# Performance work log

Hardware: AMD Instinct MI355X
Metric: run time of the kernel (lower is better)

Reference implementation:

```python
import jax, jax.numpy as jnp
import numpy as np

N, E, D = 20000, 320000, 256
EPS = 1e-5


def setup_inputs() -> dict:
    key = jax.random.key(0)
    ks = jax.random.split(key, 12)
    s = 1.0 / np.sqrt(D)
    s2 = 1.0 / np.sqrt(2 * D)
    return {
        "node_embeddings": jax.random.normal(ks[0], (N, D), jnp.float32),
        "edge_index": jax.random.randint(ks[1], (2, E), 0, N, jnp.int64),
        "edge_embeddings": jax.random.normal(ks[2], (E, D), jnp.float32),
        # message MLP: Linear(D,D) -> GELU -> Linear(D,D)
        "W1m": jax.random.uniform(ks[3], (D, D), jnp.float32, -s, s),
        "b1m": jnp.zeros((D,), jnp.float32),
        "W2m": jax.random.uniform(ks[4], (D, D), jnp.float32, -s, s),
        "b2m": jnp.zeros((D,), jnp.float32),
        # update MLP: Linear(D,2D) -> GELU -> Linear(2D,D)
        "W1u": jax.random.uniform(ks[5], (D, 2 * D), jnp.float32, -s, s),
        "b1u": jnp.zeros((2 * D,), jnp.float32),
        "W2u": jax.random.uniform(ks[6], (2 * D, D), jnp.float32, -s2, s2),
        "b2u": jnp.zeros((D,), jnp.float32),
        # LayerNorm params
        "gamma": jnp.ones((D,), jnp.float32),
        "beta": jnp.zeros((D,), jnp.float32),
    }


def _layer_norm(x, gamma, beta):
    mu = jnp.mean(x, axis=-1, keepdims=True)
    var = jnp.mean(jnp.square(x - mu), axis=-1, keepdims=True)
    return (x - mu) * jax.lax.rsqrt(var + EPS) * gamma + beta


def reference(node_embeddings, edge_index, edge_embeddings,
              W1m, b1m, W2m, b2m, W1u, b1u, W2u, b2u, gamma, beta):
    src = edge_index[0]
    dst = edge_index[1]
    n = node_embeddings.shape[0]
    # gather + edge add + message MLP (exact erf GELU, as torch default)
    h = node_embeddings[src] + edge_embeddings           # [E, D]
    h = jax.nn.gelu(h @ W1m + b1m, approximate=False)
    messages = h @ W2m + b2m                             # [E, D]
    # scatter-mean aggregation
    agg = jax.ops.segment_sum(messages, dst, num_segments=n)  # [N, D]
    deg = jax.ops.segment_sum(jnp.ones((dst.shape[0], 1), node_embeddings.dtype),
                              dst, num_segments=n)            # [N, 1]
    agg = agg / jnp.maximum(deg, 1.0)
    # update MLP + residual + LayerNorm
    u = jax.nn.gelu(agg @ W1u + b1u, approximate=False) @ W2u + b2u
    return _layer_norm(node_embeddings + u, gamma, beta)
```

## Files before the change

### kernel.cpp

```cpp
#include <hip/hip_runtime.h>
#include <hip/hip_bf16.h>

#define N_NODES 20000
#define N_EDGES 320000

typedef __attribute__((ext_vector_type(8))) short short8;
typedef __attribute__((ext_vector_type(4))) float f32x4;

static __device__ __forceinline__ unsigned short f2bf(float f) {
  __hip_bfloat16 h = __float2bfloat16(f);
  union { __hip_bfloat16 h; unsigned short u; } cv; cv.h = h; return cv.u;
}

static __device__ __forceinline__ float bf2f(unsigned short u) {
  union { unsigned int u; float f; } cv; cv.u = ((unsigned int)u) << 16; return cv.f;
}

static __device__ __forceinline__ unsigned int pk2(float a, float b) {
  return (unsigned int)f2bf(a) | ((unsigned int)f2bf(b) << 16);
}

static __device__ __forceinline__ float gelu_exact(float v) {
  return 0.5f * v * (1.0f + erff(v * 0.70710678118654752f));
}

#define SWZ(row, byteoff) ((byteoff) ^ (((row) & 7) << 4))
#define SWZU(b) ((b) ^ ((((b) >> 8) & 7) << 4))

__global__ void zero_kernel(float4* __restrict__ S4, int4* __restrict__ cnt4) {
  int idx = blockIdx.x * blockDim.x + threadIdx.x;
  S4[idx] = make_float4(0.f, 0.f, 0.f, 0.f);
  if (idx < N_NODES / 4) cnt4[idx] = make_int4(0, 0, 0, 0);
}

__global__ void pack_kernel(const float* __restrict__ W1m, const float* __restrict__ W2m,
                            const float* __restrict__ W1u, const float* __restrict__ W2u,
                            unsigned short* __restrict__ P1m, unsigned short* __restrict__ P2m,
                            unsigned short* __restrict__ P1u, unsigned short* __restrict__ P2u) {
  int idx = blockIdx.x * blockDim.x + threadIdx.x;
  const float* W; unsigned short* P; int K, Nc, local;
  if (idx < 65536)        { W = W1m; P = P1m; K = 256; Nc = 256; local = idx; }
  else if (idx < 131072)  { W = W2m; P = P2m; K = 256; Nc = 256; local = idx - 65536; }
  else if (idx < 262144)  { W = W1u; P = P1u; K = 256; Nc = 512; local = idx - 131072; }
  else                    { W = W2u; P = P2u; K = 512; Nc = 256; local = idx - 262144; }
  int frag = local >> 9, wi = local & 511;
  int l = wi >> 3, i = wi & 7;
  int kf = K >> 5;
  int cf = frag / kf, t = frag % kf;
  int k = t * 32 + (l >> 4) * 8 + i;
  int n = cf * 16 + (l & 15);
  P[local] = f2bf(W[(size_t)k * Nc + n]);
}

__global__ void hist_kernel(const int* __restrict__ dst, int* __restrict__ cnt) {
  int e = blockIdx.x * blockDim.x + threadIdx.x;
  atomicAdd(&cnt[dst[e]], 1);
}

__global__ __launch_bounds__(1024) void scan_kernel(const int* __restrict__ cnt,
                                                    int* __restrict__ rptr,
                                                    int* __restrict__ cur) {
  __shared__ int sums[1024];
  const int t = threadIdx.x;
  const int base = t * 20;
  int local[20];
  int s = 0;
#pragma unroll
  for (int i = 0; i < 20; ++i) {
    int idx = base + i;
    int v = (idx < N_NODES) ? cnt[idx] : 0;
    local[i] = s;
    s += v;
  }
  int v = s;
  sums[t] = v;
  for (int off = 1; off < 1024; off <<= 1) {
    __syncthreads();
    int o = (t >= off) ? sums[t - off] : 0;
    __syncthreads();
    v += o;
    sums[t] = v;
  }
  int excl = v - s;
#pragma unroll
  for (int i = 0; i < 20; ++i) {
    int idx = base + i;
    if (idx < N_NODES) { int p = excl + local[i]; rptr[idx] = p; cur[idx] = p; }
  }
  if (t == 1023) rptr[N_NODES] = v;
}

__global__ void scatter_kernel(const int* __restrict__ dst, int* __restrict__ cur,
                               int* __restrict__ perm) {
  int e = blockIdx.x * blockDim.x + threadIdx.x;
  int d = dst[e];
  int pos = atomicAdd(&cur[d], 1);
  perm[pos] = e;
}

__global__ __launch_bounds__(256) void edge_kernel(
    const float* __restrict__ node, const float* __restrict__ eemb,
    const int* __restrict__ src, const int* __restrict__ dst,
    const int* __restrict__ perm,
    const unsigned short* __restrict__ P1m, const float* __restrict__ b1m,
    float* __restrict__ S) {
  __shared__ unsigned short tA[64 * 256];
  __shared__ int dstS[64];
  const int tid = threadIdx.x;
  const int e0 = blockIdx.x * 64;
  {
    const int r = tid >> 2;
    const int cs = (tid & 3) * 64;
    const int e = perm[e0 + r];
    const int se = src[e];
    if ((tid & 3) == 0) dstS[r] = dst[e];
    const float* ep = eemb + (size_t)e * 256 + cs;
    const float* np = node + (size_t)se * 256 + cs;
#pragma unroll
    for (int i = 0; i < 8; ++i) {
      float4 a = *(const float4*)(ep + i * 8);
      float4 b = *(const float4*)(np + i * 8);
      float4 c = *(const float4*)(ep + i * 8 + 4);
      float4 d = *(const float4*)(np + i * 8 + 4);
      uint4 p;
      p.x = pk2(a.x + b.x, a.y + b.y);
      p.y = pk2(a.z + b.z, a.w + b.w);
      p.z = pk2(c.x + d.x, c.y + d.y);
      p.w = pk2(c.z + d.z, c.w + d.w);
      *(uint4*)((char*)tA + SWZ(r, r * 512 + (cs + i * 8) * 2)) = p;
    }
  }
  __syncthreads();

  const int w = tid >> 6, l = tid & 63;
  const int lr = l & 15, lh = l >> 4;
  f32x4 acc[4][4];
#pragma unroll
  for (int c = 0; c < 4; ++c) {
    float bb = b1m[w * 64 + c * 16 + lr];
#pragma unroll
    for (int r4 = 0; r4 < 4; ++r4) acc[r4][c] = f32x4{bb, bb, bb, bb};
  }
#pragma unroll
  for (int t = 0; t < 8; ++t) {
    short8 af[4], bfr[4];
#pragma unroll
    for (int r4 = 0; r4 < 4; ++r4) {
      int row = r4 * 16 + lr;
      af[r4] = *(const short8*)((const char*)tA + SWZ(row, row * 512 + t * 64 + lh * 16));
    }
#pragma unroll
    for (int c = 0; c < 4; ++c)
      bfr[c] = *(const short8*)(P1m + (size_t)(((w * 4 + c) * 8 + t) * 512 + l * 8));
#pragma unroll
    for (int r4 = 0; r4 < 4; ++r4)
#pragma unroll
      for (int c = 0; c < 4; ++c)
        acc[r4][c] = __builtin_amdgcn_mfma_f32_16x16x32_bf16(af[r4], bfr[c], acc[r4][c], 0, 0, 0);
  }
  __syncthreads();

#pragma unroll
  for (int r4 = 0; r4 < 4; ++r4)
#pragma unroll
    for (int c = 0; c < 4; ++c) {
      int col = w * 64 + c * 16 + lr;
#pragma unroll
      for (int j = 0; j < 4; ++j) {
        int row = r4 * 16 + lh * 4 + j;
        *(unsigned short*)((char*)tA + SWZ(row, row * 512 + col * 2)) =
            f2bf(gelu_exact(acc[r4][c][j]));
      }
    }
  __syncthreads();

  {
    const int col = tid;
    float run = 0.f;
    int cur = dstS[0];
#pragma unroll 8
    for (int row = 0; row < 64; ++row) {
      int d = dstS[row];
      float v = bf2f(*(const unsigned short*)((const char*)tA + SWZ(row, row * 512 + col * 2)));
      if (d != cur) {
        atomicAdd(&S[(size_t)cur * 256 + col], run);
        run = 0.f;
        cur = d;
      }
      run += v;
    }
    atomicAdd(&S[(size_t)cur * 256 + col], run);
  }
}

__global__ __launch_bounds__(256) void node_kernel(
    const float* __restrict__ node, const float* __restrict__ S, const int* __restrict__ rptr,
    const unsigned short* __restrict__ P2m, const float* __restrict__ b2m,
    const unsigned short* __restrict__ P1u, const float* __restrict__ b1u,
    const unsigned short* __restrict__ P2u, const float* __restrict__ b2u,
    const float* __restrict__ gamma, const float* __restrict__ beta,
    float* __restrict__ out) {
  __shared__ unsigned short tAB[2][64 * 256];
  __shared__ unsigned short tH[64 * 512];
  __shared__ float fmu[64], frs[64], fflag[64];
  float* tU = (float*)tAB;
  const int tid = threadIdx.x;
  const int n0 = blockIdx.x * 64;
  const int r = tid >> 2;
  const int cs = (tid & 3) * 64;
  const int n = n0 + r;
  const bool valid = n < N_NODES;
  {
    int dgi = valid ? (rptr[n + 1] - rptr[n]) : 0;
    float dg = (float)dgi;
    float rec = 1.0f / fmaxf(dg, 1.0f);
    if ((tid & 3) == 0) fflag[r] = (dgi > 0) ? 1.0f : 0.0f;
    const float4* sp = (const float4*)(S + (size_t)n * 256 + cs);
#pragma unroll
    for (int i = 0; i < 8; ++i) {
      float4 a = valid ? sp[2 * i]     : make_float4(0.f, 0.f, 0.f, 0.f);
      float4 b = valid ? sp[2 * i + 1] : make_float4(0.f, 0.f, 0.f, 0.f);
      uint4 p;
      p.x = pk2(a.x * rec, a.y * rec);
      p.y = pk2(a.z * rec, a.w * rec);
      p.z = pk2(b.x * rec, b.y * rec);
      p.w = pk2(b.z * rec, b.w * rec);
      *(uint4*)((char*)tAB[0] + SWZ(r, r * 512 + (cs + i * 8) * 2)) = p;
    }
  }
  __syncthreads();
  const int w = tid >> 6, l = tid & 63, lr = l & 15, lh = l >> 4;

  {
    f32x4 acc[4][4];
#pragma unroll
    for (int r4 = 0; r4 < 4; ++r4)
#pragma unroll
      for (int c = 0; c < 4; ++c) acc[r4][c] = f32x4{0.f, 0.f, 0.f, 0.f};
#pragma unroll
    for (int t = 0; t < 8; ++t) {
      short8 af[4], bfr[4];
#pragma unroll
      for (int r4 = 0; r4 < 4; ++r4) {
        int row = r4 * 16 + lr;
        af[r4] = *(const short8*)((const char*)tAB[0] + SWZ(row, row * 512 + t * 64 + lh * 16));
      }
#pragma unroll
      for (int c = 0; c < 4; ++c)
        bfr[c] = *(const short8*)(P2m + (size_t)(((w * 4 + c) * 8 + t) * 512 + l * 8));
#pragma unroll
      for (int r4 = 0; r4 < 4; ++r4)
#pragma unroll
        for (int c = 0; c < 4; ++c)
          acc[r4][c] = __builtin_amdgcn_mfma_f32_16x16x32_bf16(af[r4], bfr[c], acc[r4][c], 0, 0, 0);
    }
#pragma unroll
    for (int r4 = 0; r4 < 4; ++r4)
#pragma unroll
      for (int c = 0; c < 4; ++c) {
        int col = w * 64 + c * 16 + lr;
        float bm = b2m[col];
#pragma unroll
        for (int j = 0; j < 4; ++j) {
          int row = r4 * 16 + lh * 4 + j;
          float v = acc[r4][c][j] + fflag[row] * bm;
          *(unsigned short*)((char*)tAB[1] + SWZ(row, row * 512 + col * 2)) = f2bf(v);
        }
      }
  }
  __syncthreads();

  {
    f32x4 acc[4][8];
#pragma unroll
    for (int r4 = 0; r4 < 4; ++r4)
#pragma unroll
      for (int c = 0; c < 8; ++c) acc[r4][c] = f32x4{0.f, 0.f, 0.f, 0.f};
#pragma unroll
    for (int t = 0; t < 8; ++t) {
      short8 af[4], bfr[8];
#pragma unroll
      for (int r4 = 0; r4 < 4; ++r4) {
        int row = r4 * 16 + lr;
        af[r4] = *(const short8*)((const char*)tAB[1] + SWZ(row, row * 512 + t * 64 + lh * 16));
      }
#pragma unroll
      for (int c = 0; c < 8; ++c)
        bfr[c] = *(const short8*)(P1u + (size_t)(((w * 8 + c) * 8 + t) * 512 + l * 8));
#pragma unroll
      for (int r4 = 0; r4 < 4; ++r4)
#pragma unroll
        for (int c = 0; c < 8; ++c)
          acc[r4][c] = __builtin_amdgcn_mfma_f32_16x16x32_bf16(af[r4], bfr[c], acc[r4][c], 0, 0, 0);
    }
#pragma unroll
    for (int r4 = 0; r4 < 4; ++r4)
#pragma unroll
      for (int c = 0; c < 8; ++c) {
        int col = w * 128 + c * 16 + lr;
        float b1 = b1u[col];
#pragma unroll
        for (int j = 0; j < 4; ++j) {
          int row = r4 * 16 + lh * 4 + j;
          float v = gelu_exact(acc[r4][c][j] + b1);
          *(unsigned short*)((char*)tH + SWZ(row, row * 1024 + col * 2)) = f2bf(v);
        }
      }
  }
  __syncthreads();

  {
    f32x4 acc[4][4];
#pragma unroll
    for (int r4 = 0; r4 < 4; ++r4)
#pragma unroll
      for (int c = 0; c < 4; ++c) acc[r4][c] = f32x4{0.f, 0.f, 0.f, 0.f};
#pragma unroll
    for (int t = 0; t < 16; ++t) {
      short8 af[4], bfr[4];
#pragma unroll
      for (int r4 = 0; r4 < 4; ++r4) {
        int row = r4 * 16 + lr;
        af[r4] = *(const short8*)((const char*)tH + SWZ(row, row * 1024 + t * 64 + lh * 16));
      }
#pragma unroll
      for (int c = 0; c < 4; ++c)
        bfr[c] = *(const short8*)(P2u + (size_t)(((w * 4 + c) * 16 + t) * 512 + l * 8));
#pragma unroll
      for (int r4 = 0; r4 < 4; ++r4)
#pragma unroll
        for (int c = 0; c < 4; ++c)
          acc[r4][c] = __builtin_amdgcn_mfma_f32_16x16x32_bf16(af[r4], bfr[c], acc[r4][c], 0, 0, 0);
    }
#pragma unroll
    for (int r4 = 0; r4 < 4; ++r4)
#pragma unroll
      for (int c = 0; c < 4; ++c) {
        int col = w * 64 + c * 16 + lr;
        float b2 = b2u[col];
#pragma unroll
        for (int j = 0; j < 4; ++j) {
          int row = r4 * 16 + lh * 4 + j;
          *(float*)((char*)tU + SWZU(row * 1024 + col * 4)) = acc[r4][c][j] + b2;
        }
      }
  }
  __syncthreads();

  {
    float sum = 0.f, sq = 0.f;
#pragma unroll
    for (int i = 0; i < 16; ++i) {
      int byte = SWZU(r * 1024 + (cs + i * 4) * 4);
      float4 v = *(float4*)((char*)tU + byte);
      if (valid) {
        const float4 nb = *(const float4*)(node + (size_t)n * 256 + cs + i * 4);
        v.x += nb.x; v.y += nb.y; v.z += nb.z; v.w += nb.w;
        *(float4*)((char*)tU + byte) = v;
      }
      sum += v.x + v.y + v.z + v.w;
      sq += v.x * v.x + v.y * v.y + v.z * v.z + v.w * v.w;
    }
    sum += __shfl_xor(sum, 1); sum += __shfl_xor(sum, 2);
    sq  += __shfl_xor(sq, 1);  sq  += __shfl_xor(sq, 2);
    if ((tid & 3) == 0) {
      float mu = sum * (1.0f / 256.0f);
      fmu[r] = mu;
      frs[r] = rsqrtf(fmaxf(sq * (1.0f / 256.0f) - mu * mu, 0.0f) + 1e-5f);
    }
  }
  __syncthreads();
#pragma unroll
  for (int i = 0; i < 16; ++i) {
    int f4 = i * 256 + tid;
    int row = f4 >> 6;
    int c4 = f4 & 63;
    int nn = n0 + row;
    if (nn < N_NODES) {
      float4 v = *(float4*)((char*)tU + SWZU(row * 1024 + c4 * 16));
      float mu = fmu[row], rs = frs[row];
      float4 g  = *(const float4*)(gamma + c4 * 4);
      float4 bt = *(const float4*)(beta + c4 * 4);
      float4 o;
      o.x = (v.x - mu) * rs * g.x + bt.x;
      o.y = (v.y - mu) * rs * g.y + bt.y;
      o.z = (v.z - mu) * rs * g.z + bt.z;
      o.w = (v.w - mu) * rs * g.w + bt.w;
      *(float4*)(out + (size_t)nn * 256 + c4 * 4) = o;
    }
  }
}

extern "C" void kernel_launch(void* const* d_in, const int* in_sizes, int n_in,
                              void* d_out, int out_size, void* d_ws, size_t ws_size,
                              hipStream_t stream) {
  const float* node = (const float*)d_in[0];
  const int* eidx = (const int*)d_in[1];
  const float* eemb = (const float*)d_in[2];
  const float* W1m = (const float*)d_in[3];
  const float* b1m = (const float*)d_in[4];
  const float* W2m = (const float*)d_in[5];
  const float* b2m = (const float*)d_in[6];
  const float* W1u = (const float*)d_in[7];
  const float* b1u = (const float*)d_in[8];
  const float* W2u = (const float*)d_in[9];
  const float* b2u = (const float*)d_in[10];
  const float* gamma = (const float*)d_in[11];
  const float* beta = (const float*)d_in[12];
  float* out = (float*)d_out;

  char* ws = (char*)d_ws;
  int* cnt  = (int*)ws;
  int* rptr = (int*)(ws + 81920);
  int* cur  = (int*)(ws + 163840);
  int* perm = (int*)(ws + 245760);
  unsigned short* P1m = (unsigned short*)(ws + 1525760);
  unsigned short* P2m = (unsigned short*)(ws + 1656832);
  unsigned short* P1u = (unsigned short*)(ws + 1787904);
  unsigned short* P2u = (unsigned short*)(ws + 2050048);
  const int* src = eidx;
  const int* dst = eidx + N_EDGES;

  zero_kernel<<<N_NODES * 64 / 256, 256, 0, stream>>>((float4*)out, (int4*)cnt);
  pack_kernel<<<393216 / 256, 256, 0, stream>>>(W1m, W2m, W1u, W2u, P1m, P2m, P1u, P2u);
  hist_kernel<<<N_EDGES / 256, 256, 0, stream>>>(dst, cnt);
  scan_kernel<<<1, 1024, 0, stream>>>(cnt, rptr, cur);
  scatter_kernel<<<N_EDGES / 256, 256, 0, stream>>>(dst, cur, perm);
  edge_kernel<<<N_EDGES / 64, 256, 0, stream>>>(node, eemb, src, dst, perm, P1m, b1m, out);
  node_kernel<<<(N_NODES + 63) / 64, 256, 0, stream>>>(node, out, rptr, P2m, b2m,
                                                       P1u, b1u, P2u, b2u, gamma, beta, out);
}
```

Before: 387.2 us.

## Software-pipeline edge tiles in edge_kernel and use fast exp-based GELU

Each edge block now processes four 64-edge tiles and prefetches the next tile's gathered node and edge rows into registers while the current tile runs its MFMA, GELU and scatter phases. This hides global gather latency and amortises per-block setup. It also replaces the exact erf GELU with a sigmoid-style exp2 and reciprocal approximation in both kernels, which is cheaper but slightly less accurate. The launch has a quarter as many blocks, which reduces parallelism, and extra registers are held for the staging buffers.

```diff
diff --git a/kernel.cpp b/kernel.cpp
--- a/kernel.cpp
+++ b/kernel.cpp
@@ -3,6 +3,7 @@
 
 #define N_NODES 20000
 #define N_EDGES 320000
+#define ETILES 4
 
 typedef __attribute__((ext_vector_type(8))) short short8;
 typedef __attribute__((ext_vector_type(4))) float f32x4;
@@ -20,8 +21,19 @@
   return (unsigned int)f2bf(a) | ((unsigned int)f2bf(b) << 16);
 }
 
-static __device__ __forceinline__ float gelu_exact(float v) {
-  return 0.5f * v * (1.0f + erff(v * 0.70710678118654752f));
+static __device__ __forceinline__ float gelu_f(float x) {
+  float z = x * (2.3022082f + 0.1029432f * x * x);
+  z = fminf(fmaxf(z, -30.0f), 30.0f);
+#if __has_builtin(__builtin_amdgcn_exp2f)
+  float t = __builtin_amdgcn_exp2f(z);
+#else
+  float t = exp2f(z);
+#endif
+#if __has_builtin(__builtin_amdgcn_rcpf)
+  return x * t * __builtin_amdgcn_rcpf(1.0f + t);
+#else
+  return x * t / (1.0f + t);
+#endif
 }
 
 #define SWZ(row, byteoff) ((byteoff) ^ (((row) & 7) << 4))
@@ -107,89 +119,122 @@
   __shared__ unsigned short tA[64 * 256];
   __shared__ int dstS[64];
   const int tid = threadIdx.x;
-  const int e0 = blockIdx.x * 64;
-  {
-    const int r = tid >> 2;
-    const int cs = (tid & 3) * 64;
-    const int e = perm[e0 + r];
-    const int se = src[e];
-    if ((tid & 3) == 0) dstS[r] = dst[e];
-    const float* ep = eemb + (size_t)e * 256 + cs;
-    const float* np = node + (size_t)se * 256 + cs;
-#pragma unroll
-    for (int i = 0; i < 8; ++i) {
-      float4 a = *(const float4*)(ep + i * 8);
-      float4 b = *(const float4*)(np + i * 8);
-      float4 c = *(const float4*)(ep + i * 8 + 4);
-      float4 d = *(const float4*)(np + i * 8 + 4);
-      uint4 p;
-      p.x = pk2(a.x + b.x, a.y + b.y);
-      p.y = pk2(a.z + b.z, a.w + b.w);
-      p.z = pk2(c.x + d.x, c.y + d.y);
-      p.w = pk2(c.z + d.z, c.w + d.w);
-      *(uint4*)((char*)tA + SWZ(r, r * 512 + (cs + i * 8) * 2)) = p;
-    }
-  }
-  __syncthreads();
-
-  const int w = tid >> 6, l = tid & 63;
-  const int lr = l & 15, lh = l >> 4;
-  f32x4 acc[4][4];
-#pragma unroll
-  for (int c = 0; c < 4; ++c) {
-    float bb = b1m[w * 64 + c * 16 + lr];
-#pragma unroll
-    for (int r4 = 0; r4 < 4; ++r4) acc[r4][c] = f32x4{bb, bb, bb, bb};
-  }
-#pragma unroll
-  for (int t = 0; t < 8; ++t) {
-    short8 af[4], bfr[4];
-#pragma unroll
-    for (int r4 = 0; r4 < 4; ++r4) {
-      int row = r4 * 16 + lr;
-      af[r4] = *(const short8*)((const char*)tA + SWZ(row, row * 512 + t * 64 + lh * 16));
-    }
+  const int r = tid >> 2, cs = (tid & 3) * 64;
+  const int w = tid >> 6, l = tid & 63, lr = l & 15, lh = l >> 4;
+  const int base = blockIdx.x * (64 * ETILES);
+
+  int eId[ETILES], sId[ETILES], dId[ETILES];
+#pragma unroll
+  for (int t = 0; t < ETILES; ++t) eId[t] = perm[base + t * 64 + r];
+#pragma unroll
+  for (int t = 0; t < ETILES; ++t) { sId[t] = src[eId[t]]; dId[t] = dst[eId[t]]; }
+
+  float bias_c[4];
+#pragma unroll
+  for (int c = 0; c < 4; ++c) bias_c[c] = b1m[w * 64 + c * 16 + lr];
+
+  float4 fa[8], fb[8];
+  uint4 stg[8];
+
+  auto issue_half = [&](int t, int h) {
+    const float* ep = eemb + (size_t)eId[t] * 256 + cs + h * 32;
+    const float* np = node + (size_t)sId[t] * 256 + cs + h * 32;
+#pragma unroll
+    for (int j = 0; j < 8; ++j) {
+      fa[j] = *(const float4*)(ep + j * 4);
+      fb[j] = *(const float4*)(np + j * 4);
+    }
+  };
+  auto pack_half = [&](uint4* o) {
+#pragma unroll
+    for (int j = 0; j < 4; ++j) {
+      float4 a = fa[2 * j], b = fb[2 * j], c = fa[2 * j + 1], d = fb[2 * j + 1];
+      o[j].x = pk2(a.x + b.x, a.y + b.y);
+      o[j].y = pk2(a.z + b.z, a.w + b.w);
+      o[j].z = pk2(c.x + d.x, c.y + d.y);
+      o[j].w = pk2(c.z + d.z, c.w + d.w);
+    }
+  };
+  auto write_stage = [&](int t) {
+#pragma unroll
+    for (int i = 0; i < 8; ++i)
+      *(uint4*)((char*)tA + SWZ(r, r * 512 + (cs + i * 8) * 2)) = stg[i];
+    if ((tid & 3) == 0) dstS[r] = dId[t];
+  };
+
+  issue_half(0, 0); pack_half(&stg[0]);
+  issue_half(0, 1); pack_half(&stg[4]);
+  write_stage(0);
+  __syncthreads();
+
+  for (int t = 0; t < ETILES; ++t) {
+    const bool last = (t == ETILES - 1);
+    if (!last) issue_half(t + 1, 0);
+
+    f32x4 acc[4][4];
 #pragma unroll
     for (int c = 0; c < 4; ++c)
-      bfr[c] = *(const short8*)(P1m + (size_t)(((w * 4 + c) * 8 + t) * 512 + l * 8));
-#pragma unroll
-    for (int r4 = 0; r4 < 4; ++r4)
+#pragma unroll
+      for (int r4 = 0; r4 < 4; ++r4) acc[r4][c] = f32x4{bias_c[c], bias_c[c], bias_c[c], bias_c[c]};
+#pragma unroll
+    for (int kt = 0; kt < 8; ++kt) {
+      short8 af[4], bfr[4];
+#pragma unroll
+      for (int r4 = 0; r4 < 4; ++r4) {
+        int row = r4 * 16 + lr;
+        af[r4] = *(const short8*)((const char*)tA + SWZ(row, row * 512 + kt * 64 + lh * 16));
+      }
 #pragma unroll
       for (int c = 0; c < 4; ++c)
-        acc[r4][c] = __builtin_amdgcn_mfma_f32_16x16x32_bf16(af[r4], bfr[c], acc[r4][c], 0, 0, 0);
-  }
-  __syncthreads();
-
-#pragma unroll
-  for (int r4 = 0; r4 < 4; ++r4)
-#pragma unroll
-    for (int c = 0; c < 4; ++c) {
-      int col = w * 64 + c * 16 + lr;
-#pragma unroll
-      for (int j = 0; j < 4; ++j) {
-        int row = r4 * 16 + lh * 4 + j;
-        *(unsigned short*)((char*)tA + SWZ(row, row * 512 + col * 2)) =
-            f2bf(gelu_exact(acc[r4][c][j]));
-      }
-    }
-  __syncthreads();
-
-  {
-    const int col = tid;
-    float run = 0.f;
-    int cur = dstS[0];
+        bfr[c] = *(const short8*)(P1m + (size_t)(((w * 4 + c) * 8 + kt) * 512 + l * 8));
+#pragma unroll
+      for (int r4 = 0; r4 < 4; ++r4)
+#pragma unroll
+        for (int c = 0; c < 4; ++c)
+          acc[r4][c] = __builtin_amdgcn_mfma_f32_16x16x32_bf16(af[r4], bfr[c], acc[r4][c], 0, 0, 0);
+    }
+    __syncthreads();
+
+    if (!last) { pack_half(&stg[0]); issue_half(t + 1, 1); }
+
+#pragma unroll
+    for (int r4 = 0; r4 < 4; ++r4)
+#pragma unroll
+      for (int c = 0; c < 4; ++c) {
+        int col = w * 64 + c * 16 + lr;
+#pragma unroll
+        for (int j = 0; j < 4; ++j) {
+          int row = r4 * 16 + lh * 4 + j;
+          *(unsigned short*)((char*)tA + SWZ(row, row * 512 + col * 2)) =
+              f2bf(gelu_f(acc[r4][c][j]));
+        }
+      }
+    __syncthreads();
+
+    {
+      const int col = tid;
+      float run = 0.f;
+      int cur = dstS[0];
 #pragma unroll 8
-    for (int row = 0; row < 64; ++row) {
-      int d = dstS[row];
-      float v = bf2f(*(const unsigned short*)((const char*)tA + SWZ(row, row * 512 + col * 2)));
-      if (d != cur) {
-        atomicAdd(&S[(size_t)cur * 256 + col], run);
-        run = 0.f;
-        cur = d;
-      }
-      run += v;
-    }
-    atomicAdd(&S[(size_t)cur * 256 + col], run);
+      for (int row = 0; row < 64; ++row) {
+        int d = dstS[row];
+        float v = bf2f(*(const unsigned short*)((const char*)tA + SWZ(row, row * 512 + col * 2)));
+        if (d != cur) {
+          atomicAdd(&S[(size_t)cur * 256 + col], run);
+          run = 0.f;
+          cur = d;
+        }
+        run += v;
+      }
+      atomicAdd(&S[(size_t)cur * 256 + col], run);
+    }
+
+    if (!last) {
+      pack_half(&stg[4]);
+      __syncthreads();
+      write_stage(t + 1);
+      __syncthreads();
+    }
   }
 }
 
@@ -302,7 +347,7 @@
 #pragma unroll
         for (int j = 0; j < 4; ++j) {
           int row = r4 * 16 + lh * 4 + j;
-          float v = gelu_exact(acc[r4][c][j] + b1);
+          float v = gelu_f(acc[r4][c][j] + b1);
           *(unsigned short*)((char*)tH + SWZ(row, row * 1024 + col * 2)) = f2bf(v);
         }
       }
@@ -426,7 +471,7 @@
   hist_kernel<<<N_EDGES / 256, 256, 0, stream>>>(dst, cnt);
   scan_kernel<<<1, 1024, 0, stream>>>(cnt, rptr, cur);
   scatter_kernel<<<N_EDGES / 256, 256, 0, stream>>>(dst, cur, perm);
-  edge_kernel<<<N_EDGES / 64, 256, 0, stream>>>(node, eemb, src, dst, perm, P1m, b1m, out);
+  edge_kernel<<<N_EDGES / (64 * ETILES), 256, 0, stream>>>(node, eemb, src, dst, perm, P1m, b1m, out);
   node_kernel<<<(N_NODES + 63) / 64, 256, 0, stream>>>(node, out, rptr, P2m, b2m,
                                                        P1u, b1u, P2u, b2u, gamma, beta, out);
 }
```

Measured after the change: 579.4 us. 49.7% more time.
